# Optimization experiments

Measured on AMD Instinct MI355X. Metric: run time of the kernel, lower is better.

Reference implementation:

```python
import jax, jax.numpy as jnp
import numpy as np

SWIGLU_ALPHA = 1.702
SWIGLU_LIMIT = 7.0
B, S, H, E, K, I = 2, 2048, 2048, 32, 4, 1024


def setup_inputs() -> dict:
    key = jax.random.key(0)
    ks = jax.random.split(key, 8)
    return {
        "hidden_states": jax.random.normal(ks[0], (B, S, H), jnp.float32),
        "gate_w": jax.random.normal(ks[1], (E, H), jnp.float32) * 0.02,
        "gate_b": jnp.zeros((E,), jnp.float32),
        "w_gate": jax.random.normal(ks[2], (E, H, I), jnp.float32) * 0.02,
        "b_gate": jnp.zeros((E, I), jnp.float32),
        "w_up": jax.random.normal(ks[3], (E, H, I), jnp.float32) * 0.02,
        "b_up": jnp.zeros((E, I), jnp.float32),
        "w_down": jax.random.normal(ks[4], (E, I, H), jnp.float32) * 0.02,
        "b_down": jnp.zeros((E, H), jnp.float32),
    }


def reference(hidden_states, gate_w, gate_b, w_gate, b_gate, w_up, b_up, w_down, b_down):
    Bb, Ss, Hh = hidden_states.shape
    x = hidden_states.reshape(-1, Hh)                      # [T, H]
    # --- gate: top-k logits first, then softmax over the selected subset ---
    logits = x @ gate_w.T + gate_b                         # [T, E]
    topk_logits, topk_idx = jax.lax.top_k(logits, K)       # sorted descending
    topk_weight = jax.nn.softmax(topk_logits.astype(jnp.float32), axis=-1)  # [T, K]
    # --- dispatch: replicate each token K times, sort by expert id ---
    flat_idx = topk_idx.reshape(-1)                        # [T*K]
    xs = jnp.repeat(x, K, axis=0)                          # [T*K, H]
    order = jnp.argsort(flat_idx)                          # stable sort by expert
    xt = xs[order]
    gid = flat_idx[order]                                  # expert id per sorted row
    group_sizes = jnp.bincount(flat_idx, length=E).astype(jnp.int32)
    # --- grouped GEMM experts with GPT-OSS SwiGLU ---
    gate = jax.lax.ragged_dot(xt, w_gate, group_sizes) + b_gate[gid]
    up = jax.lax.ragged_dot(xt, w_up, group_sizes) + b_up[gid]
    gate = jnp.minimum(gate, SWIGLU_LIMIT)
    up = jnp.clip(up, -SWIGLU_LIMIT, SWIGLU_LIMIT)
    glu = gate * jax.nn.sigmoid(SWIGLU_ALPHA * gate)
    activated = (up + 1.0) * glu
    outs = jax.lax.ragged_dot(activated, w_down, group_sizes) + b_down[gid]
    # --- unsort and combine with routing weights ---
    inv = jnp.argsort(order)
    outs = outs[inv].reshape(-1, K, Hh)                    # [T, K, H]
    y = jnp.sum(outs * topk_weight[..., None], axis=1).astype(x.dtype)
    return y.reshape(Bb, Ss, Hh)
```

## Files before the change

### kernel.cpp

```cpp
#include <hip/hip_runtime.h>

#define T_TOK 4096
#define E_EXP 32
#define HDIM  2048
#define IDIM  1024
#define TKROW 16384
#define BM    256
#define MAXT  96

typedef __attribute__((ext_vector_type(8))) short   short8;
typedef __attribute__((ext_vector_type(8))) __bf16  bf16x8;
typedef __attribute__((ext_vector_type(4))) float   f32x4;

typedef const __attribute__((address_space(1))) unsigned int* gas_t;
typedef __attribute__((address_space(3))) unsigned int*       las_t;

static __device__ __forceinline__ void gload16(const void* g, void* l) {
    __builtin_amdgcn_global_load_lds((gas_t)(uintptr_t)g, (las_t)(uintptr_t)l, 16, 0, 0);
}

static __device__ __forceinline__ f32x4 mfma16(short8 a, short8 b, f32x4 c) {
    return __builtin_amdgcn_mfma_f32_16x16x32_bf16(
        __builtin_bit_cast(bf16x8, a), __builtin_bit_cast(bf16x8, b), c, 0, 0, 0);
}

static __device__ __forceinline__ unsigned short f2bf(float f) {
    unsigned u = __builtin_bit_cast(unsigned, f);
    unsigned r = (u + 0x7FFFu + ((u >> 16) & 1u)) >> 16;
    return (unsigned short)r;
}
static __device__ __forceinline__ float bf2f(unsigned short u) {
    return __builtin_bit_cast(float, ((unsigned)u) << 16);
}
static __device__ __forceinline__ unsigned cvtpk(float lo, float hi) {
    unsigned r;
    asm("v_cvt_pk_bf16_f32 %0, %1, %2" : "=v"(r) : "v"(lo), "v"(hi));
    return r;
}

#define VM0()   asm volatile("s_waitcnt vmcnt(0)" ::: "memory")
#define LGKM0() asm volatile("s_waitcnt lgkmcnt(0)" ::: "memory")

__global__ __launch_bounds__(256) void gating_kernel(
    const float* __restrict__ x, const float* __restrict__ gw,
    const float* __restrict__ gb, int* __restrict__ topk_idx,
    float* __restrict__ topk_w)
{
    int wave = threadIdx.x >> 6, lane = threadIdx.x & 63;
    int t = blockIdx.x * 4 + wave;
    const float* xr = x + (size_t)t * HDIM;
    float xv[32];
#pragma unroll
    for (int j = 0; j < 32; j++) xv[j] = xr[lane + 64 * j];
    float logits[E_EXP];
#pragma unroll
    for (int e = 0; e < E_EXP; e++) {
        const float* wr = gw + (size_t)e * HDIM;
        float s = 0.f;
#pragma unroll
        for (int j = 0; j < 32; j++) s = fmaf(xv[j], wr[lane + 64 * j], s);
#pragma unroll
        for (int off = 32; off; off >>= 1) s += __shfl_xor(s, off);
        logits[e] = s + gb[e];
    }
    unsigned sel = 0;
    float v[4]; int id[4];
#pragma unroll
    for (int kk = 0; kk < 4; kk++) {
        float best = -3.4e38f; int bi = 0;
#pragma unroll
        for (int e = 0; e < E_EXP; e++) {
            bool ok = ((sel >> e) & 1u) == 0u;
            bool gt = ok && (logits[e] > best);
            best = gt ? logits[e] : best;
            bi   = gt ? e : bi;
        }
        sel |= 1u << bi; v[kk] = best; id[kk] = bi;
    }
    float m0 = v[0];
    float e0 = __expf(v[0] - m0), e1 = __expf(v[1] - m0);
    float e2 = __expf(v[2] - m0), e3 = __expf(v[3] - m0);
    float inv = 1.f / (e0 + e1 + e2 + e3);
    if (lane == 0) {
        int b4 = t * 4;
        topk_idx[b4 + 0] = id[0]; topk_w[b4 + 0] = e0 * inv;
        topk_idx[b4 + 1] = id[1]; topk_w[b4 + 1] = e1 * inv;
        topk_idx[b4 + 2] = id[2]; topk_w[b4 + 2] = e2 * inv;
        topk_idx[b4 + 3] = id[3]; topk_w[b4 + 3] = e3 * inv;
    }
}

__global__ void init_kernel(int* counts, int* fill) {
    if (threadIdx.x < E_EXP) { counts[threadIdx.x] = 0; fill[threadIdx.x] = 0; }
}

__global__ void histo_kernel(const int* __restrict__ idx, int* counts) {
    int i = blockIdx.x * 256 + threadIdx.x;
    atomicAdd(&counts[idx[i]], 1);
}

__global__ void scan_tiles_kernel(const int* counts, int* offsets,
                                  int* tile_e, int* tile_r, int* ntiles) {
    if (threadIdx.x == 0) {
        int acc = 0;
        for (int e = 0; e < E_EXP; e++) { offsets[e] = acc; acc += counts[e]; }
        offsets[E_EXP] = acc;
        int nt = 0;
        for (int e = 0; e < E_EXP; e++) {
            int c = counts[e];
            for (int r = 0; r < c; r += BM) {
                tile_e[nt] = e; tile_r[nt] = offsets[e] + r; nt++;
            }
        }
        ntiles[0] = nt;
    }
}

__global__ void scatter_kernel(const int* __restrict__ idx, const int* __restrict__ offsets,
                               int* fill, int* __restrict__ pos_of, int* __restrict__ row_tok) {
    int i = blockIdx.x * 256 + threadIdx.x;
    int e = idx[i];
    int pos = offsets[e] + atomicAdd(&fill[e], 1);
    pos_of[i] = pos;
    row_tok[pos] = i >> 2;
}

__global__ __launch_bounds__(64) void gather_kernel(
    const float* __restrict__ x, const int* __restrict__ row_tok,
    unsigned short* __restrict__ xt)
{
    int r = blockIdx.x, lane = threadIdx.x;
    const f32x4* src = (const f32x4*)(x + (size_t)row_tok[r] * HDIM);
    unsigned short* dst = xt + (size_t)r * HDIM;
#pragma unroll
    for (int j = 0; j < 8; j++) {
        f32x4 f = src[lane + 64 * j];
        uint2 o;
        o.x = cvtpk(f[0], f[1]);
        o.y = cvtpk(f[2], f[3]);
        *(uint2*)(dst + 4 * (lane + 64 * j)) = o;
    }
}

__global__ __launch_bounds__(512, 2) void gemm1_kernel(
    const unsigned short* __restrict__ xt, const float* __restrict__ w_gate,
    const float* __restrict__ b_gate, const float* __restrict__ w_up,
    const float* __restrict__ b_up, const int* __restrict__ tile_e,
    const int* __restrict__ tile_r, const int* __restrict__ ntiles,
    const int* __restrict__ offsets, const int* __restrict__ counts,
    unsigned short* __restrict__ act)
{
    int flat = blockIdx.y * 8 + blockIdx.x;
    int swz = (flat & 7) * (MAXT * 8 / 8) + (flat >> 3);
    int tid = swz >> 3, nb = swz & 7;
    if (tid >= ntiles[0]) return;
    int e = tile_e[tid], row0 = tile_r[tid];
    int cnt_end = offsets[e] + counts[e];
    int n0 = nb * 128;

    __shared__ unsigned short As[2][BM * 64];
    __shared__ unsigned short Bgs[2][128 * 64];
    __shared__ unsigned short Bus[2][128 * 64];

    int t = threadIdx.x, lane = t & 63, w = t >> 6;
    int wr = w >> 2, wc = w & 3;
    int lrow = lane & 15, lg8 = (lane >> 4) * 8;

    f32x4 accg[8][2], accu[8][2];
#pragma unroll
    for (int m = 0; m < 8; m++)
#pragma unroll
        for (int n = 0; n < 2; n++) { accg[m][n] = (f32x4)0.f; accu[m][n] = (f32x4)0.f; }

    int arow_l = (lane >> 3);
    int achunk = (lane & 7) ^ arow_l;
    int bn = (t & 31) * 4, bk = (t >> 5) * 4;
    int bfswz = ((t & 31) & 7) << 3;
    size_t wB = (size_t)e * ((size_t)HDIM * IDIM) + (size_t)bk * IDIM + n0 + bn;

    f32x4 gReg[4], uReg[4];

#define G1_STAGE_A(KT, BUF) do { int k0_ = (KT) * 64; \
    _Pragma("unroll") for (int i_ = 0; i_ < 4; i_++) { \
        int ar_ = row0 + 32 * w + 8 * i_ + arow_l; \
        if (ar_ > TKROW - 1) ar_ = TKROW - 1; \
        gload16(xt + (size_t)ar_ * HDIM + k0_ + achunk * 8, \
                (void*)&As[BUF][(32 * w + 8 * i_) * 64]); \
    } } while (0)

#define G1_LOADB(KT) do { \
    const float* gp_ = w_gate + wB + (size_t)(KT) * 64 * IDIM; \
    const float* up_ = w_up   + wB + (size_t)(KT) * 64 * IDIM; \
    _Pragma("unroll") for (int kk_ = 0; kk_ < 4; kk_++) { \
        gReg[kk_] = *(const f32x4*)(gp_ + (size_t)kk_ * IDIM); \
        uReg[kk_] = *(const f32x4*)(up_ + (size_t)kk_ * IDIM); \
    } } while (0)

#define G1_WRITEB(BUF) do { \
    _Pragma("unroll") for (int j_ = 0; j_ < 4; j_++) { \
        uint2 vg_, vu_; \
        vg_.x = cvtpk(gReg[0][j_], gReg[1][j_]); vg_.y = cvtpk(gReg[2][j_], gReg[3][j_]); \
        vu_.x = cvtpk(uReg[0][j_], uReg[1][j_]); vu_.y = cvtpk(uReg[2][j_], uReg[3][j_]); \
        int d_ = (bn + j_) * 64 + (bk ^ bfswz); \
        *(uint2*)&Bgs[BUF][d_] = vg_; *(uint2*)&Bus[BUF][d_] = vu_; \
    } } while (0)

#define G1_MFMA(BUF) do { \
    __builtin_amdgcn_s_setprio(1); \
    _Pragma("unroll") for (int kk_ = 0; kk_ < 2; kk_++) { \
        short8 af_[8], bg_[2], bu_[2]; \
        int ke_ = kk_ * 32 + lg8; \
        _Pragma("unroll") for (int m_ = 0; m_ < 8; m_++) \
            af_[m_] = *(const short8*)&As[BUF][(wr * 128 + m_ * 16 + lrow) * 64 + (ke_ ^ ((lrow & 7) << 3))]; \
        _Pragma("unroll") for (int n_ = 0; n_ < 2; n_++) { \
            int rb_ = wc * 32 + n_ * 16 + lrow; \
            int d_ = rb_ * 64 + (ke_ ^ (((rb_ >> 2) & 7) << 3)); \
            bg_[n_] = *(const short8*)&Bgs[BUF][d_]; \
            bu_[n_] = *(const short8*)&Bus[BUF][d_]; \
        } \
        _Pragma("unroll") for (int m_ = 0; m_ < 8; m_++) \
        _Pragma("unroll") for (int n_ = 0; n_ < 2; n_++) { \
            accg[m_][n_] = mfma16(af_[m_], bg_[n_], accg[m_][n_]); \
            accu[m_][n_] = mfma16(af_[m_], bu_[n_], accu[m_][n_]); \
        } \
    } \
    __builtin_amdgcn_s_setprio(0); } while (0)

    G1_STAGE_A(0, 0);
    G1_LOADB(0);
    VM0();
    G1_WRITEB(0);
    LGKM0();
    __builtin_amdgcn_s_barrier();

    int cur = 0;
#pragma unroll 1
    for (int kt = 0; kt < 32; kt++) {
        if (kt + 1 < 32) { G1_STAGE_A(kt + 1, cur ^ 1); G1_LOADB(kt + 1); }
        G1_MFMA(cur);
        VM0();
        if (kt + 1 < 32) G1_WRITEB(cur ^ 1);
        LGKM0();
        __builtin_amdgcn_s_barrier();
        cur ^= 1;
    }
#undef G1_STAGE_A
#undef G1_LOADB
#undef G1_WRITEB
#undef G1_MFMA

#pragma unroll
    for (int nf = 0; nf < 2; nf++) {
        int col = n0 + wc * 32 + nf * 16 + lrow;
        float bgv = b_gate[e * IDIM + col];
        float buv = b_up[e * IDIM + col];
#pragma unroll
        for (int m = 0; m < 8; m++) {
            int rb = row0 + wr * 128 + m * 16 + (lane >> 4) * 4;
#pragma unroll
            for (int r = 0; r < 4; r++) {
                int grow = rb + r;
                if (grow < cnt_end) {
                    float gv = accg[m][nf][r] + bgv;
                    float uv = accu[m][nf][r] + buv;
                    gv = fminf(gv, 7.f);
                    uv = fminf(fmaxf(uv, -7.f), 7.f);
                    float glu = gv / (1.f + __expf(-1.702f * gv));
                    act[(size_t)grow * IDIM + col] = f2bf((uv + 1.f) * glu);
                }
            }
        }
    }
}

__global__ __launch_bounds__(512, 2) void gemm2_kernel(
    const unsigned short* __restrict__ actb, const float* __restrict__ w_down,
    const float* __restrict__ b_down, const int* __restrict__ tile_e,
    const int* __restrict__ tile_r, const int* __restrict__ ntiles,
    const int* __restrict__ offsets, const int* __restrict__ counts,
    unsigned short* __restrict__ outs)
{
    int flat = blockIdx.y * 8 + blockIdx.x;
    int swz = (flat & 7) * (MAXT * 8 / 8) + (flat >> 3);
    int tid = swz >> 3, nb = swz & 7;
    if (tid >= ntiles[0]) return;
    int e = tile_e[tid], row0 = tile_r[tid];
    int cnt_end = offsets[e] + counts[e];
    int n0 = nb * 256;

    __shared__ unsigned short As[2][BM * 64];
    __shared__ unsigned short Bs[2][256 * 64];

    int t = threadIdx.x, lane = t & 63, w = t >> 6;
    int wr = w >> 2, wc = w & 3;
    int lrow = lane & 15, lg8 = (lane >> 4) * 8;

    f32x4 acc[8][4];
#pragma unroll
    for (int m = 0; m < 8; m++)
#pragma unroll
        for (int n = 0; n < 4; n++) acc[m][n] = (f32x4)0.f;

    int arow_l = (lane >> 3);
    int achunk = (lane & 7) ^ arow_l;
    int bn = (t & 63) * 4, bk = w * 8;
    int bfswz = (lane & 7) << 3;
    size_t wB = (size_t)e * ((size_t)IDIM * HDIM) + (size_t)bk * HDIM + n0 + bn;

    f32x4 dReg[8];

#define G2_STAGE_A(KT, BUF) do { int k0_ = (KT) * 64; \
    _Pragma("unroll") for (int i_ = 0; i_ < 4; i_++) { \
        int ar_ = row0 + 32 * w + 8 * i_ + arow_l; \
        if (ar_ > TKROW - 1) ar_ = TKROW - 1; \
        gload16(actb + (size_t)ar_ * IDIM + k0_ + achunk * 8, \
                (void*)&As[BUF][(32 * w + 8 * i_) * 64]); \
    } } while (0)

#define G2_LOADB(KT) do { \
    const float* gp_ = w_down + wB + (size_t)(KT) * 64 * HDIM; \
    _Pragma("unroll") for (int kk_ = 0; kk_ < 8; kk_++) \
        dReg[kk_] = *(const f32x4*)(gp_ + (size_t)kk_ * HDIM); \
    } while (0)

#define G2_WRITEB(BUF) do { \
    _Pragma("unroll") for (int j_ = 0; j_ < 4; j_++) { \
        uint4 v_; \
        v_.x = cvtpk(dReg[0][j_], dReg[1][j_]); v_.y = cvtpk(dReg[2][j_], dReg[3][j_]); \
        v_.z = cvtpk(dReg[4][j_], dReg[5][j_]); v_.w = cvtpk(dReg[6][j_], dReg[7][j_]); \
        int d_ = (bn + j_) * 64 + (bk ^ bfswz); \
        *(uint4*)&Bs[BUF][d_] = v_; \
    } } while (0)

#define G2_MFMA(BUF) do { \
    __builtin_amdgcn_s_setprio(1); \
    _Pragma("unroll") for (int kk_ = 0; kk_ < 2; kk_++) { \
        short8 af_[8], bf_[4]; \
        int ke_ = kk_ * 32 + lg8; \
        _Pragma("unroll") for (int m_ = 0; m_ < 8; m_++) \
            af_[m_] = *(const short8*)&As[BUF][(wr * 128 + m_ * 16 + lrow) * 64 + (ke_ ^ ((lrow & 7) << 3))]; \
        _Pragma("unroll") for (int n_ = 0; n_ < 4; n_++) { \
            int rb_ = wc * 64 + n_ * 16 + lrow; \
            bf_[n_] = *(const short8*)&Bs[BUF][rb_ * 64 + (ke_ ^ (((rb_ >> 2) & 7) << 3))]; \
        } \
        _Pragma("unroll") for (int m_ = 0; m_ < 8; m_++) \
        _Pragma("unroll") for (int n_ = 0; n_ < 4; n_++) \
            acc[m_][n_] = mfma16(af_[m_], bf_[n_], acc[m_][n_]); \
    } \
    __builtin_amdgcn_s_setprio(0); } while (0)

    G2_STAGE_A(0, 0);
    G2_LOADB(0);
    VM0();
    G2_WRITEB(0);
    LGKM0();
    __builtin_amdgcn_s_barrier();

    int cur = 0;
#pragma unroll 1
    for (int kt = 0; kt < 16; kt++) {
        if (kt + 1 < 16) { G2_STAGE_A(kt + 1, cur ^ 1); G2_LOADB(kt + 1); }
        G2_MFMA(cur);
        VM0();
        if (kt + 1 < 16) G2_WRITEB(cur ^ 1);
        LGKM0();
        __builtin_amdgcn_s_barrier();
        cur ^= 1;
    }
#undef G2_STAGE_A
#undef G2_LOADB
#undef G2_WRITEB
#undef G2_MFMA

#pragma unroll
    for (int nf = 0; nf < 4; nf++) {
        int col = n0 + wc * 64 + nf * 16 + lrow;
        float bdv = b_down[e * HDIM + col];
#pragma unroll
        for (int m = 0; m < 8; m++) {
            int rb = row0 + wr * 128 + m * 16 + (lane >> 4) * 4;
#pragma unroll
            for (int r = 0; r < 4; r++) {
                int grow = rb + r;
                if (grow < cnt_end)
                    outs[(size_t)grow * HDIM + col] = f2bf(acc[m][nf][r] + bdv);
            }
        }
    }
}

__global__ __launch_bounds__(256) void combine_kernel(
    const unsigned short* __restrict__ outs, const int* __restrict__ pos_of,
    const float* __restrict__ topk_w, float* __restrict__ y)
{
    int tok = blockIdx.x;
    int c0 = threadIdx.x * 8;
    float acc[8] = {0.f, 0.f, 0.f, 0.f, 0.f, 0.f, 0.f, 0.f};
#pragma unroll
    for (int k = 0; k < 4; k++) {
        int pos = pos_of[tok * 4 + k];
        float w = topk_w[tok * 4 + k];
        short8 vv = *(const short8*)(outs + (size_t)pos * HDIM + c0);
#pragma unroll
        for (int j = 0; j < 8; j++)
            acc[j] = fmaf(w, bf2f((unsigned short)vv[j]), acc[j]);
    }
    float4 o0 = make_float4(acc[0], acc[1], acc[2], acc[3]);
    float4 o1 = make_float4(acc[4], acc[5], acc[6], acc[7]);
    *(float4*)(y + (size_t)tok * HDIM + c0)     = o0;
    *(float4*)(y + (size_t)tok * HDIM + c0 + 4) = o1;
}

extern "C" void kernel_launch(void* const* d_in, const int* in_sizes, int n_in,
                              void* d_out, int out_size, void* d_ws, size_t ws_size,
                              hipStream_t stream) {
    const float* x      = (const float*)d_in[0];
    const float* gw     = (const float*)d_in[1];
    const float* gb     = (const float*)d_in[2];
    const float* w_gate = (const float*)d_in[3];
    const float* b_gate = (const float*)d_in[4];
    const float* w_up   = (const float*)d_in[5];
    const float* b_up   = (const float*)d_in[6];
    const float* w_down = (const float*)d_in[7];
    const float* b_down = (const float*)d_in[8];
    float* y = (float*)d_out;

    char* base = (char*)d_ws;
    size_t off = 0;
    int*   topk_idx = (int*)(base + off);   off += (size_t)TKROW * 4;
    float* topk_w   = (float*)(base + off); off += (size_t)TKROW * 4;
    int*   counts   = (int*)(base + off);   off += 256;
    int*   offsets  = (int*)(base + off);   off += 256;
    int*   fill     = (int*)(base + off);   off += 256;
    int*   ntiles   = (int*)(base + off);   off += 256;
    int*   tile_e   = (int*)(base + off);   off += 1024;
    int*   tile_r   = (int*)(base + off);   off += 1024;
    int*   pos_of   = (int*)(base + off);   off += (size_t)TKROW * 4;
    int*   row_tok  = (int*)(base + off);   off += (size_t)TKROW * 4;
    unsigned short* xt   = (unsigned short*)(base + off); off += (size_t)TKROW * HDIM * 2;
    unsigned short* act  = (unsigned short*)(base + off); off += (size_t)TKROW * IDIM * 2;
    unsigned short* outs = (unsigned short*)(base + off); off += (size_t)TKROW * HDIM * 2;

    init_kernel<<<1, 64, 0, stream>>>(counts, fill);
    gating_kernel<<<T_TOK / 4, 256, 0, stream>>>(x, gw, gb, topk_idx, topk_w);
    histo_kernel<<<TKROW / 256, 256, 0, stream>>>(topk_idx, counts);
    scan_tiles_kernel<<<1, 64, 0, stream>>>(counts, offsets, tile_e, tile_r, ntiles);
    scatter_kernel<<<TKROW / 256, 256, 0, stream>>>(topk_idx, offsets, fill, pos_of, row_tok);
    gather_kernel<<<TKROW, 64, 0, stream>>>(x, row_tok, xt);
    gemm1_kernel<<<dim3(8, MAXT), 512, 0, stream>>>(
        xt, w_gate, b_gate, w_up, b_up, tile_e, tile_r, ntiles, offsets, counts, act);
    gemm2_kernel<<<dim3(8, MAXT), 512, 0, stream>>>(
        act, w_down, b_down, tile_e, tile_r, ntiles, offsets, counts, outs);
    combine_kernel<<<T_TOK, 256, 0, stream>>>(outs, pos_of, topk_w, y);
}
```

Measured before the change: 622.6 us.

## Stage fp32 expert weights directly to LDS and halve row tile size

Both grouped GEMMs now load fp32 weight tiles straight into shared memory with global_load_lds and convert them to bf16 while building MFMA fragments, replacing the register-staged load, convert and LDS write path. The M tile shrinks from 256 to 128 rows and the K step from 64 to 32, raising occupancy to 4 blocks per CU and reducing padding waste for ragged expert groups. In exchange, weights are read from LDS as scalar fp32 values with repeated conversion per wave, LDS traffic rises, and the tile count and barrier count double.

```diff
diff --git a/kernel.cpp b/kernel.cpp
--- a/kernel.cpp
+++ b/kernel.cpp
@@ -5,8 +5,8 @@
 #define HDIM  2048
 #define IDIM  1024
 #define TKROW 16384
-#define BM    256
-#define MAXT  96
+#define BM    128
+#define MAXT  160
 
 typedef __attribute__((ext_vector_type(8))) short   short8;
 typedef __attribute__((ext_vector_type(8))) __bf16  bf16x8;
@@ -37,9 +37,16 @@
     asm("v_cvt_pk_bf16_f32 %0, %1, %2" : "=v"(r) : "v"(lo), "v"(hi));
     return r;
 }
+static __device__ __forceinline__ short8 pack8(float v0, float v1, float v2, float v3,
+                                               float v4, float v5, float v6, float v7) {
+    uint4 u;
+    u.x = cvtpk(v0, v1); u.y = cvtpk(v2, v3);
+    u.z = cvtpk(v4, v5); u.w = cvtpk(v6, v7);
+    return __builtin_bit_cast(short8, u);
+}
 
 #define VM0()   asm volatile("s_waitcnt vmcnt(0)" ::: "memory")
-#define LGKM0() asm volatile("s_waitcnt lgkmcnt(0)" ::: "memory")
+#define BAR()   do { __builtin_amdgcn_s_barrier(); __builtin_amdgcn_sched_barrier(0); } while (0)
 
 __global__ __launch_bounds__(256) void gating_kernel(
     const float* __restrict__ x, const float* __restrict__ gw,
@@ -142,7 +149,7 @@
     }
 }
 
-__global__ __launch_bounds__(512, 2) void gemm1_kernel(
+__global__ __launch_bounds__(512, 4) void gemm1_kernel(
     const unsigned short* __restrict__ xt, const float* __restrict__ w_gate,
     const float* __restrict__ b_gate, const float* __restrict__ w_up,
     const float* __restrict__ b_up, const int* __restrict__ tile_e,
@@ -151,102 +158,80 @@
     unsigned short* __restrict__ act)
 {
     int flat = blockIdx.y * 8 + blockIdx.x;
-    int swz = (flat & 7) * (MAXT * 8 / 8) + (flat >> 3);
+    int swz = (flat & 7) * MAXT + (flat >> 3);
     int tid = swz >> 3, nb = swz & 7;
     if (tid >= ntiles[0]) return;
     int e = tile_e[tid], row0 = tile_r[tid];
     int cnt_end = offsets[e] + counts[e];
     int n0 = nb * 128;
 
-    __shared__ unsigned short As[2][BM * 64];
-    __shared__ unsigned short Bgs[2][128 * 64];
-    __shared__ unsigned short Bus[2][128 * 64];
+    __shared__ unsigned short As[2][BM * 32];
+    __shared__ float Bg[2][32 * 128];
+    __shared__ float Bu[2][32 * 128];
 
     int t = threadIdx.x, lane = t & 63, w = t >> 6;
     int wr = w >> 2, wc = w & 3;
-    int lrow = lane & 15, lg8 = (lane >> 4) * 8;
-
-    f32x4 accg[8][2], accu[8][2];
-#pragma unroll
-    for (int m = 0; m < 8; m++)
+    int lrow = lane & 15;
+    int kf8 = (lane >> 4) * 8;
+
+    f32x4 accg[4][2], accu[4][2];
+#pragma unroll
+    for (int m = 0; m < 4; m++)
 #pragma unroll
         for (int n = 0; n < 2; n++) { accg[m][n] = (f32x4)0.f; accu[m][n] = (f32x4)0.f; }
 
-    int arow_l = (lane >> 3);
-    int achunk = (lane & 7) ^ arow_l;
-    int bn = (t & 31) * 4, bk = (t >> 5) * 4;
-    int bfswz = ((t & 31) & 7) << 3;
-    size_t wB = (size_t)e * ((size_t)HDIM * IDIM) + (size_t)bk * IDIM + n0 + bn;
-
-    f32x4 gReg[4], uReg[4];
-
-#define G1_STAGE_A(KT, BUF) do { int k0_ = (KT) * 64; \
-    _Pragma("unroll") for (int i_ = 0; i_ < 4; i_++) { \
-        int ar_ = row0 + 32 * w + 8 * i_ + arow_l; \
-        if (ar_ > TKROW - 1) ar_ = TKROW - 1; \
-        gload16(xt + (size_t)ar_ * HDIM + k0_ + achunk * 8, \
-                (void*)&As[BUF][(32 * w + 8 * i_) * 64]); \
+    int arow = row0 + 16 * w + (lane >> 2);
+    if (arow > TKROW - 1) arow = TKROW - 1;
+    const unsigned short* aSrc = xt + (size_t)arow * HDIM + (lane & 3) * 8;
+    size_t eBase = (size_t)e * ((size_t)HDIM * IDIM);
+    const float* gSrc = w_gate + eBase + (size_t)(4 * w + (lane >> 5)) * IDIM + n0 + (lane & 31) * 4;
+    const float* uSrc = w_up   + eBase + (size_t)(4 * w + (lane >> 5)) * IDIM + n0 + (lane & 31) * 4;
+
+#define G1_STAGE(KT, BUF) do { \
+    gload16(aSrc + (size_t)(KT) * 32, (void*)&As[BUF][(16 * w) * 32]); \
+    _Pragma("unroll") for (int i_ = 0; i_ < 2; i_++) { \
+        size_t ko_ = (size_t)(KT) * 32 * IDIM + (size_t)(2 * i_) * IDIM; \
+        gload16(gSrc + ko_, (void*)&Bg[BUF][(4 * w + 2 * i_) * 128]); \
+        gload16(uSrc + ko_, (void*)&Bu[BUF][(4 * w + 2 * i_) * 128]); \
     } } while (0)
 
-#define G1_LOADB(KT) do { \
-    const float* gp_ = w_gate + wB + (size_t)(KT) * 64 * IDIM; \
-    const float* up_ = w_up   + wB + (size_t)(KT) * 64 * IDIM; \
-    _Pragma("unroll") for (int kk_ = 0; kk_ < 4; kk_++) { \
-        gReg[kk_] = *(const f32x4*)(gp_ + (size_t)kk_ * IDIM); \
-        uReg[kk_] = *(const f32x4*)(up_ + (size_t)kk_ * IDIM); \
-    } } while (0)
-
-#define G1_WRITEB(BUF) do { \
-    _Pragma("unroll") for (int j_ = 0; j_ < 4; j_++) { \
-        uint2 vg_, vu_; \
-        vg_.x = cvtpk(gReg[0][j_], gReg[1][j_]); vg_.y = cvtpk(gReg[2][j_], gReg[3][j_]); \
-        vu_.x = cvtpk(uReg[0][j_], uReg[1][j_]); vu_.y = cvtpk(uReg[2][j_], uReg[3][j_]); \
-        int d_ = (bn + j_) * 64 + (bk ^ bfswz); \
-        *(uint2*)&Bgs[BUF][d_] = vg_; *(uint2*)&Bus[BUF][d_] = vu_; \
-    } } while (0)
-
 #define G1_MFMA(BUF) do { \
+    const unsigned short* Ab_ = &As[BUF][0]; \
+    const float* Bgb_ = &Bg[BUF][0]; const float* Bub_ = &Bu[BUF][0]; \
+    short8 bgf_[2], buf_[2]; \
+    _Pragma("unroll") for (int nf_ = 0; nf_ < 2; nf_++) { \
+        int nc_ = wc * 32 + nf_ * 16 + lrow; \
+        bgf_[nf_] = pack8(Bgb_[(kf8 + 0) * 128 + nc_], Bgb_[(kf8 + 1) * 128 + nc_], \
+                          Bgb_[(kf8 + 2) * 128 + nc_], Bgb_[(kf8 + 3) * 128 + nc_], \
+                          Bgb_[(kf8 + 4) * 128 + nc_], Bgb_[(kf8 + 5) * 128 + nc_], \
+                          Bgb_[(kf8 + 6) * 128 + nc_], Bgb_[(kf8 + 7) * 128 + nc_]); \
+        buf_[nf_] = pack8(Bub_[(kf8 + 0) * 128 + nc_], Bub_[(kf8 + 1) * 128 + nc_], \
+                          Bub_[(kf8 + 2) * 128 + nc_], Bub_[(kf8 + 3) * 128 + nc_], \
+                          Bub_[(kf8 + 4) * 128 + nc_], Bub_[(kf8 + 5) * 128 + nc_], \
+                          Bub_[(kf8 + 6) * 128 + nc_], Bub_[(kf8 + 7) * 128 + nc_]); \
+    } \
     __builtin_amdgcn_s_setprio(1); \
-    _Pragma("unroll") for (int kk_ = 0; kk_ < 2; kk_++) { \
-        short8 af_[8], bg_[2], bu_[2]; \
-        int ke_ = kk_ * 32 + lg8; \
-        _Pragma("unroll") for (int m_ = 0; m_ < 8; m_++) \
-            af_[m_] = *(const short8*)&As[BUF][(wr * 128 + m_ * 16 + lrow) * 64 + (ke_ ^ ((lrow & 7) << 3))]; \
-        _Pragma("unroll") for (int n_ = 0; n_ < 2; n_++) { \
-            int rb_ = wc * 32 + n_ * 16 + lrow; \
-            int d_ = rb_ * 64 + (ke_ ^ (((rb_ >> 2) & 7) << 3)); \
-            bg_[n_] = *(const short8*)&Bgs[BUF][d_]; \
-            bu_[n_] = *(const short8*)&Bus[BUF][d_]; \
-        } \
-        _Pragma("unroll") for (int m_ = 0; m_ < 8; m_++) \
-        _Pragma("unroll") for (int n_ = 0; n_ < 2; n_++) { \
-            accg[m_][n_] = mfma16(af_[m_], bg_[n_], accg[m_][n_]); \
-            accu[m_][n_] = mfma16(af_[m_], bu_[n_], accu[m_][n_]); \
+    _Pragma("unroll") for (int m_ = 0; m_ < 4; m_++) { \
+        int rr_ = wr * 64 + m_ * 16 + lrow; \
+        short8 af_ = *(const short8*)&Ab_[rr_ * 32 + kf8]; \
+        _Pragma("unroll") for (int nf_ = 0; nf_ < 2; nf_++) { \
+            accg[m_][nf_] = mfma16(af_, bgf_[nf_], accg[m_][nf_]); \
+            accu[m_][nf_] = mfma16(af_, buf_[nf_], accu[m_][nf_]); \
         } \
     } \
     __builtin_amdgcn_s_setprio(0); } while (0)
 
-    G1_STAGE_A(0, 0);
-    G1_LOADB(0);
-    VM0();
-    G1_WRITEB(0);
-    LGKM0();
-    __builtin_amdgcn_s_barrier();
-
+    G1_STAGE(0, 0);
+    VM0(); BAR();
     int cur = 0;
 #pragma unroll 1
-    for (int kt = 0; kt < 32; kt++) {
-        if (kt + 1 < 32) { G1_STAGE_A(kt + 1, cur ^ 1); G1_LOADB(kt + 1); }
+    for (int kt = 0; kt < 64; kt++) {
+        if (kt + 1 < 64) G1_STAGE(kt + 1, cur ^ 1);
         G1_MFMA(cur);
-        VM0();
-        if (kt + 1 < 32) G1_WRITEB(cur ^ 1);
-        LGKM0();
-        __builtin_amdgcn_s_barrier();
+        VM0(); BAR();
         cur ^= 1;
     }
-#undef G1_STAGE_A
-#undef G1_LOADB
-#undef G1_WRITEB
+#undef G1_STAGE
 #undef G1_MFMA
 
 #pragma unroll
@@ -255,8 +240,8 @@
         float bgv = b_gate[e * IDIM + col];
         float buv = b_up[e * IDIM + col];
 #pragma unroll
-        for (int m = 0; m < 8; m++) {
-            int rb = row0 + wr * 128 + m * 16 + (lane >> 4) * 4;
+        for (int m = 0; m < 4; m++) {
+            int rb = row0 + wr * 64 + m * 16 + (lane >> 4) * 4;
 #pragma unroll
             for (int r = 0; r < 4; r++) {
                 int grow = rb + r;
@@ -273,7 +258,7 @@
     }
 }
 
-__global__ __launch_bounds__(512, 2) void gemm2_kernel(
+__global__ __launch_bounds__(512, 4) void gemm2_kernel(
     const unsigned short* __restrict__ actb, const float* __restrict__ w_down,
     const float* __restrict__ b_down, const int* __restrict__ tile_e,
     const int* __restrict__ tile_r, const int* __restrict__ ntiles,
@@ -281,95 +266,71 @@
     unsigned short* __restrict__ outs)
 {
     int flat = blockIdx.y * 8 + blockIdx.x;
-    int swz = (flat & 7) * (MAXT * 8 / 8) + (flat >> 3);
+    int swz = (flat & 7) * MAXT + (flat >> 3);
     int tid = swz >> 3, nb = swz & 7;
     if (tid >= ntiles[0]) return;
     int e = tile_e[tid], row0 = tile_r[tid];
     int cnt_end = offsets[e] + counts[e];
     int n0 = nb * 256;
 
-    __shared__ unsigned short As[2][BM * 64];
-    __shared__ unsigned short Bs[2][256 * 64];
+    __shared__ unsigned short As[2][BM * 32];
+    __shared__ float Bs[2][32 * 256];
 
     int t = threadIdx.x, lane = t & 63, w = t >> 6;
     int wr = w >> 2, wc = w & 3;
-    int lrow = lane & 15, lg8 = (lane >> 4) * 8;
-
-    f32x4 acc[8][4];
-#pragma unroll
-    for (int m = 0; m < 8; m++)
+    int lrow = lane & 15;
+    int kf8 = (lane >> 4) * 8;
+
+    f32x4 acc[4][4];
+#pragma unroll
+    for (int m = 0; m < 4; m++)
 #pragma unroll
         for (int n = 0; n < 4; n++) acc[m][n] = (f32x4)0.f;
 
-    int arow_l = (lane >> 3);
-    int achunk = (lane & 7) ^ arow_l;
-    int bn = (t & 63) * 4, bk = w * 8;
-    int bfswz = (lane & 7) << 3;
-    size_t wB = (size_t)e * ((size_t)IDIM * HDIM) + (size_t)bk * HDIM + n0 + bn;
-
-    f32x4 dReg[8];
-
-#define G2_STAGE_A(KT, BUF) do { int k0_ = (KT) * 64; \
+    int arow = row0 + 16 * w + (lane >> 2);
+    if (arow > TKROW - 1) arow = TKROW - 1;
+    const unsigned short* aSrc = actb + (size_t)arow * IDIM + (lane & 3) * 8;
+    const float* dSrc = w_down + (size_t)e * ((size_t)IDIM * HDIM)
+                        + (size_t)(4 * w) * HDIM + n0 + lane * 4;
+
+#define G2_STAGE(KT, BUF) do { \
+    gload16(aSrc + (size_t)(KT) * 32, (void*)&As[BUF][(16 * w) * 32]); \
     _Pragma("unroll") for (int i_ = 0; i_ < 4; i_++) { \
-        int ar_ = row0 + 32 * w + 8 * i_ + arow_l; \
-        if (ar_ > TKROW - 1) ar_ = TKROW - 1; \
-        gload16(actb + (size_t)ar_ * IDIM + k0_ + achunk * 8, \
-                (void*)&As[BUF][(32 * w + 8 * i_) * 64]); \
+        gload16(dSrc + (size_t)(KT) * 32 * HDIM + (size_t)i_ * HDIM, \
+                (void*)&Bs[BUF][(4 * w + i_) * 256]); \
     } } while (0)
 
-#define G2_LOADB(KT) do { \
-    const float* gp_ = w_down + wB + (size_t)(KT) * 64 * HDIM; \
-    _Pragma("unroll") for (int kk_ = 0; kk_ < 8; kk_++) \
-        dReg[kk_] = *(const f32x4*)(gp_ + (size_t)kk_ * HDIM); \
-    } while (0)
-
-#define G2_WRITEB(BUF) do { \
-    _Pragma("unroll") for (int j_ = 0; j_ < 4; j_++) { \
-        uint4 v_; \
-        v_.x = cvtpk(dReg[0][j_], dReg[1][j_]); v_.y = cvtpk(dReg[2][j_], dReg[3][j_]); \
-        v_.z = cvtpk(dReg[4][j_], dReg[5][j_]); v_.w = cvtpk(dReg[6][j_], dReg[7][j_]); \
-        int d_ = (bn + j_) * 64 + (bk ^ bfswz); \
-        *(uint4*)&Bs[BUF][d_] = v_; \
-    } } while (0)
-
 #define G2_MFMA(BUF) do { \
+    const unsigned short* Ab_ = &As[BUF][0]; \
+    const float* Bb_ = &Bs[BUF][0]; \
+    short8 bf_[4]; \
+    _Pragma("unroll") for (int nf_ = 0; nf_ < 4; nf_++) { \
+        int nc_ = wc * 64 + nf_ * 16 + lrow; \
+        bf_[nf_] = pack8(Bb_[(kf8 + 0) * 256 + nc_], Bb_[(kf8 + 1) * 256 + nc_], \
+                         Bb_[(kf8 + 2) * 256 + nc_], Bb_[(kf8 + 3) * 256 + nc_], \
+                         Bb_[(kf8 + 4) * 256 + nc_], Bb_[(kf8 + 5) * 256 + nc_], \
+                         Bb_[(kf8 + 6) * 256 + nc_], Bb_[(kf8 + 7) * 256 + nc_]); \
+    } \
     __builtin_amdgcn_s_setprio(1); \
-    _Pragma("unroll") for (int kk_ = 0; kk_ < 2; kk_++) { \
-        short8 af_[8], bf_[4]; \
-        int ke_ = kk_ * 32 + lg8; \
-        _Pragma("unroll") for (int m_ = 0; m_ < 8; m_++) \
-            af_[m_] = *(const short8*)&As[BUF][(wr * 128 + m_ * 16 + lrow) * 64 + (ke_ ^ ((lrow & 7) << 3))]; \
-        _Pragma("unroll") for (int n_ = 0; n_ < 4; n_++) { \
-            int rb_ = wc * 64 + n_ * 16 + lrow; \
-            bf_[n_] = *(const short8*)&Bs[BUF][rb_ * 64 + (ke_ ^ (((rb_ >> 2) & 7) << 3))]; \
-        } \
-        _Pragma("unroll") for (int m_ = 0; m_ < 8; m_++) \
-        _Pragma("unroll") for (int n_ = 0; n_ < 4; n_++) \
-            acc[m_][n_] = mfma16(af_[m_], bf_[n_], acc[m_][n_]); \
+    _Pragma("unroll") for (int m_ = 0; m_ < 4; m_++) { \
+        int rr_ = wr * 64 + m_ * 16 + lrow; \
+        short8 af_ = *(const short8*)&Ab_[rr_ * 32 + kf8]; \
+        _Pragma("unroll") for (int nf_ = 0; nf_ < 4; nf_++) \
+            acc[m_][nf_] = mfma16(af_, bf_[nf_], acc[m_][nf_]); \
     } \
     __builtin_amdgcn_s_setprio(0); } while (0)
 
-    G2_STAGE_A(0, 0);
-    G2_LOADB(0);
-    VM0();
-    G2_WRITEB(0);
-    LGKM0();
-    __builtin_amdgcn_s_barrier();
-
+    G2_STAGE(0, 0);
+    VM0(); BAR();
     int cur = 0;
 #pragma unroll 1
-    for (int kt = 0; kt < 16; kt++) {
-        if (kt + 1 < 16) { G2_STAGE_A(kt + 1, cur ^ 1); G2_LOADB(kt + 1); }
+    for (int kt = 0; kt < 32; kt++) {
+        if (kt + 1 < 32) G2_STAGE(kt + 1, cur ^ 1);
         G2_MFMA(cur);
-        VM0();
-        if (kt + 1 < 16) G2_WRITEB(cur ^ 1);
-        LGKM0();
-        __builtin_amdgcn_s_barrier();
+        VM0(); BAR();
         cur ^= 1;
     }
-#undef G2_STAGE_A
-#undef G2_LOADB
-#undef G2_WRITEB
+#undef G2_STAGE
 #undef G2_MFMA
 
 #pragma unroll
@@ -377,8 +338,8 @@
         int col = n0 + wc * 64 + nf * 16 + lrow;
         float bdv = b_down[e * HDIM + col];
 #pragma unroll
-        for (int m = 0; m < 8; m++) {
-            int rb = row0 + wr * 128 + m * 16 + (lane >> 4) * 4;
+        for (int m = 0; m < 4; m++) {
+            int rb = row0 + wr * 64 + m * 16 + (lane >> 4) * 4;
 #pragma unroll
             for (int r = 0; r < 4; r++) {
                 int grow = rb + r;
```

After: 668.4 us. 1.07x slower.

## Software-pipeline both expert GEMMs with split phases and halve gemm2 N-tile

Applied to the files above, without the earlier changes.

Both grouped GEMM kernels are restructured so each K-step is split into several barrier-separated phases that interleave LDS fragment reads, MFMA bursts, global prefetches and the bf16 conversion into shared memory. Weight registers are double-buffered two K-steps ahead, and partial vmcnt waits replace full drains. The intent is to hide global-load latency behind MFMA work instead of stalling each iteration. gemm2 also moves from 256-wide to 128-wide N tiles with twice the grid, which cuts per-block registers and LDS and adds parallelism, at the cost of reloading the A tile twice as often and paying more barriers per step.

```diff
diff --git a/kernel.cpp b/kernel.cpp
--- a/kernel.cpp
+++ b/kernel.cpp
@@ -38,8 +38,15 @@
     return r;
 }
 
-#define VM0()   asm volatile("s_waitcnt vmcnt(0)" ::: "memory")
-#define LGKM0() asm volatile("s_waitcnt lgkmcnt(0)" ::: "memory")
+#define FENCE()    asm volatile("" ::: "memory")
+#define WAITVM(N)  asm volatile("s_waitcnt vmcnt(" #N ")" ::: "memory")
+#define LGKM0()    asm volatile("s_waitcnt lgkmcnt(0)" ::: "memory")
+#define PHASE_SYNC() do { \
+    __builtin_amdgcn_s_barrier(); \
+    asm volatile("s_waitcnt lgkmcnt(0)" ::: "memory"); \
+    __builtin_amdgcn_sched_barrier(0); \
+} while (0)
+#define ENDP() do { __builtin_amdgcn_s_barrier(); __builtin_amdgcn_sched_barrier(0); } while (0)
 
 __global__ __launch_bounds__(256) void gating_kernel(
     const float* __restrict__ x, const float* __restrict__ gw,
@@ -151,7 +158,7 @@
     unsigned short* __restrict__ act)
 {
     int flat = blockIdx.y * 8 + blockIdx.x;
-    int swz = (flat & 7) * (MAXT * 8 / 8) + (flat >> 3);
+    int swz = (flat & 7) * 96 + (flat >> 3);
     int tid = swz >> 3, nb = swz & 7;
     if (tid >= ntiles[0]) return;
     int e = tile_e[tid], row0 = tile_r[tid];
@@ -178,7 +185,7 @@
     int bfswz = ((t & 31) & 7) << 3;
     size_t wB = (size_t)e * ((size_t)HDIM * IDIM) + (size_t)bk * IDIM + n0 + bn;
 
-    f32x4 gReg[4], uReg[4];
+    f32x4 gS0[4], uS0[4], gS1[4], uS1[4];
 
 #define G1_STAGE_A(KT, BUF) do { int k0_ = (KT) * 64; \
     _Pragma("unroll") for (int i_ = 0; i_ < 4; i_++) { \
@@ -188,66 +195,87 @@
                 (void*)&As[BUF][(32 * w + 8 * i_) * 64]); \
     } } while (0)
 
-#define G1_LOADB(KT) do { \
+#define G1_LOADB(KT, GV, UV) do { \
     const float* gp_ = w_gate + wB + (size_t)(KT) * 64 * IDIM; \
     const float* up_ = w_up   + wB + (size_t)(KT) * 64 * IDIM; \
     _Pragma("unroll") for (int kk_ = 0; kk_ < 4; kk_++) { \
-        gReg[kk_] = *(const f32x4*)(gp_ + (size_t)kk_ * IDIM); \
-        uReg[kk_] = *(const f32x4*)(up_ + (size_t)kk_ * IDIM); \
-    } } while (0)
-
-#define G1_WRITEB(BUF) do { \
+        GV[kk_] = *(const f32x4*)(gp_ + (size_t)kk_ * IDIM); \
+        UV[kk_] = *(const f32x4*)(up_ + (size_t)kk_ * IDIM); \
+    } } while (0)
+
+#define G1_WRITEB(GV, UV, BUF) do { \
     _Pragma("unroll") for (int j_ = 0; j_ < 4; j_++) { \
         uint2 vg_, vu_; \
-        vg_.x = cvtpk(gReg[0][j_], gReg[1][j_]); vg_.y = cvtpk(gReg[2][j_], gReg[3][j_]); \
-        vu_.x = cvtpk(uReg[0][j_], uReg[1][j_]); vu_.y = cvtpk(uReg[2][j_], uReg[3][j_]); \
+        vg_.x = cvtpk(GV[0][j_], GV[1][j_]); vg_.y = cvtpk(GV[2][j_], GV[3][j_]); \
+        vu_.x = cvtpk(UV[0][j_], UV[1][j_]); vu_.y = cvtpk(UV[2][j_], UV[3][j_]); \
         int d_ = (bn + j_) * 64 + (bk ^ bfswz); \
         *(uint2*)&Bgs[BUF][d_] = vg_; *(uint2*)&Bus[BUF][d_] = vu_; \
     } } while (0)
 
-#define G1_MFMA(BUF) do { \
+#define G1_RD_A(AF, CUR, MH, KK) do { \
+    _Pragma("unroll") for (int m_ = 0; m_ < 4; m_++) { \
+        int rr_ = wr * 128 + ((MH) * 4 + m_) * 16 + lrow; \
+        AF[m_] = *(const short8*)&As[CUR][rr_ * 64 + (((KK) * 32 + lg8) ^ ((lrow & 7) << 3))]; \
+    } } while (0)
+
+#define G1_RD_B(BG, BU, CUR, KK) do { \
+    _Pragma("unroll") for (int n_ = 0; n_ < 2; n_++) { \
+        int rb_ = wc * 32 + n_ * 16 + lrow; \
+        int d_ = rb_ * 64 + (((KK) * 32 + lg8) ^ (((rb_ >> 2) & 7) << 3)); \
+        BG[n_] = *(const short8*)&Bgs[CUR][d_]; \
+        BU[n_] = *(const short8*)&Bus[CUR][d_]; \
+    } } while (0)
+
+#define G1_MFMA16(AF, BG, BU, MH) do { \
     __builtin_amdgcn_s_setprio(1); \
-    _Pragma("unroll") for (int kk_ = 0; kk_ < 2; kk_++) { \
-        short8 af_[8], bg_[2], bu_[2]; \
-        int ke_ = kk_ * 32 + lg8; \
-        _Pragma("unroll") for (int m_ = 0; m_ < 8; m_++) \
-            af_[m_] = *(const short8*)&As[BUF][(wr * 128 + m_ * 16 + lrow) * 64 + (ke_ ^ ((lrow & 7) << 3))]; \
-        _Pragma("unroll") for (int n_ = 0; n_ < 2; n_++) { \
-            int rb_ = wc * 32 + n_ * 16 + lrow; \
-            int d_ = rb_ * 64 + (ke_ ^ (((rb_ >> 2) & 7) << 3)); \
-            bg_[n_] = *(const short8*)&Bgs[BUF][d_]; \
-            bu_[n_] = *(const short8*)&Bus[BUF][d_]; \
-        } \
-        _Pragma("unroll") for (int m_ = 0; m_ < 8; m_++) \
-        _Pragma("unroll") for (int n_ = 0; n_ < 2; n_++) { \
-            accg[m_][n_] = mfma16(af_[m_], bg_[n_], accg[m_][n_]); \
-            accu[m_][n_] = mfma16(af_[m_], bu_[n_], accu[m_][n_]); \
-        } \
+    _Pragma("unroll") for (int m_ = 0; m_ < 4; m_++) \
+    _Pragma("unroll") for (int n_ = 0; n_ < 2; n_++) { \
+        accg[(MH) * 4 + m_][n_] = mfma16(AF[m_], BG[n_], accg[(MH) * 4 + m_][n_]); \
+        accu[(MH) * 4 + m_][n_] = mfma16(AF[m_], BU[n_], accu[(MH) * 4 + m_][n_]); \
     } \
     __builtin_amdgcn_s_setprio(0); } while (0)
 
-    G1_STAGE_A(0, 0);
-    G1_LOADB(0);
-    VM0();
-    G1_WRITEB(0);
+#define G1_ITER(T, CUR, LG, LU, WG, WU) do { \
+    short8 af_[4], bg_[2], bu_[2]; \
+     \
+    G1_RD_A(af_, CUR, 0, 0); G1_RD_B(bg_, bu_, CUR, 0); \
+    if ((T) + 1 < 32) { FENCE(); G1_STAGE_A((T) + 1, (CUR) ^ 1); FENCE(); } \
+    PHASE_SYNC(); G1_MFMA16(af_, bg_, bu_, 0); ENDP(); \
+     \
+    G1_RD_A(af_, CUR, 1, 0); \
+    if ((T) + 2 < 32) { FENCE(); G1_LOADB((T) + 2, LG, LU); FENCE(); } \
+    PHASE_SYNC(); G1_MFMA16(af_, bg_, bu_, 1); ENDP(); \
+     \
+    G1_RD_A(af_, CUR, 0, 1); G1_RD_B(bg_, bu_, CUR, 1); \
+    if ((T) + 2 < 32) { WAITVM(12); } else if ((T) + 1 < 32) { WAITVM(4); } \
+    if ((T) + 1 < 32) G1_WRITEB(WG, WU, (CUR) ^ 1); \
+    PHASE_SYNC(); G1_MFMA16(af_, bg_, bu_, 0); ENDP(); \
+     \
+    G1_RD_A(af_, CUR, 1, 1); \
+    if ((T) + 2 < 32) { WAITVM(8); } else { WAITVM(0); } \
+    PHASE_SYNC(); G1_MFMA16(af_, bg_, bu_, 1); ENDP(); \
+} while (0)
+
+    G1_LOADB(0, gS0, uS0); FENCE();
+    G1_STAGE_A(0, 0); FENCE();
+    G1_LOADB(1, gS1, uS1); FENCE();
+    WAITVM(8);
+    G1_WRITEB(gS0, uS0, 0);
     LGKM0();
     __builtin_amdgcn_s_barrier();
 
-    int cur = 0;
 #pragma unroll 1
-    for (int kt = 0; kt < 32; kt++) {
-        if (kt + 1 < 32) { G1_STAGE_A(kt + 1, cur ^ 1); G1_LOADB(kt + 1); }
-        G1_MFMA(cur);
-        VM0();
-        if (kt + 1 < 32) G1_WRITEB(cur ^ 1);
-        LGKM0();
-        __builtin_amdgcn_s_barrier();
-        cur ^= 1;
+    for (int kt = 0; kt < 32; kt += 2) {
+        G1_ITER(kt,     0, gS0, uS0, gS1, uS1);
+        G1_ITER(kt + 1, 1, gS1, uS1, gS0, uS0);
     }
 #undef G1_STAGE_A
 #undef G1_LOADB
 #undef G1_WRITEB
-#undef G1_MFMA
+#undef G1_RD_A
+#undef G1_RD_B
+#undef G1_MFMA16
+#undef G1_ITER
 
 #pragma unroll
     for (int nf = 0; nf < 2; nf++) {
@@ -280,34 +308,34 @@
     const int* __restrict__ offsets, const int* __restrict__ counts,
     unsigned short* __restrict__ outs)
 {
-    int flat = blockIdx.y * 8 + blockIdx.x;
-    int swz = (flat & 7) * (MAXT * 8 / 8) + (flat >> 3);
-    int tid = swz >> 3, nb = swz & 7;
+    int flat = blockIdx.y * 16 + blockIdx.x;
+    int swz = (flat & 7) * 192 + (flat >> 3);
+    int tid = swz >> 4, nb = swz & 15;
     if (tid >= ntiles[0]) return;
     int e = tile_e[tid], row0 = tile_r[tid];
     int cnt_end = offsets[e] + counts[e];
-    int n0 = nb * 256;
+    int n0 = nb * 128;
 
     __shared__ unsigned short As[2][BM * 64];
-    __shared__ unsigned short Bs[2][256 * 64];
+    __shared__ unsigned short Bs[2][128 * 64];
 
     int t = threadIdx.x, lane = t & 63, w = t >> 6;
     int wr = w >> 2, wc = w & 3;
     int lrow = lane & 15, lg8 = (lane >> 4) * 8;
 
-    f32x4 acc[8][4];
+    f32x4 acc[8][2];
 #pragma unroll
     for (int m = 0; m < 8; m++)
 #pragma unroll
-        for (int n = 0; n < 4; n++) acc[m][n] = (f32x4)0.f;
+        for (int n = 0; n < 2; n++) acc[m][n] = (f32x4)0.f;
 
     int arow_l = (lane >> 3);
     int achunk = (lane & 7) ^ arow_l;
-    int bn = (t & 63) * 4, bk = w * 8;
-    int bfswz = (lane & 7) << 3;
+    int bn = (t & 31) * 4, bk = (t >> 5) * 4;
+    int bfswz = ((t & 31) & 7) << 3;
     size_t wB = (size_t)e * ((size_t)IDIM * HDIM) + (size_t)bk * HDIM + n0 + bn;
 
-    f32x4 dReg[8];
+    f32x4 dS0[4], dS1[4];
 
 #define G2_STAGE_A(KT, BUF) do { int k0_ = (KT) * 64; \
     _Pragma("unroll") for (int i_ = 0; i_ < 4; i_++) { \
@@ -317,64 +345,78 @@
                 (void*)&As[BUF][(32 * w + 8 * i_) * 64]); \
     } } while (0)
 
-#define G2_LOADB(KT) do { \
+#define G2_LOADB(KT, DV) do { \
     const float* gp_ = w_down + wB + (size_t)(KT) * 64 * HDIM; \
-    _Pragma("unroll") for (int kk_ = 0; kk_ < 8; kk_++) \
-        dReg[kk_] = *(const f32x4*)(gp_ + (size_t)kk_ * HDIM); \
+    _Pragma("unroll") for (int kk_ = 0; kk_ < 4; kk_++) \
+        DV[kk_] = *(const f32x4*)(gp_ + (size_t)kk_ * HDIM); \
     } while (0)
 
-#define G2_WRITEB(BUF) do { \
+#define G2_WRITEB(DV, BUF) do { \
     _Pragma("unroll") for (int j_ = 0; j_ < 4; j_++) { \
-        uint4 v_; \
-        v_.x = cvtpk(dReg[0][j_], dReg[1][j_]); v_.y = cvtpk(dReg[2][j_], dReg[3][j_]); \
-        v_.z = cvtpk(dReg[4][j_], dReg[5][j_]); v_.w = cvtpk(dReg[6][j_], dReg[7][j_]); \
+        uint2 v_; \
+        v_.x = cvtpk(DV[0][j_], DV[1][j_]); v_.y = cvtpk(DV[2][j_], DV[3][j_]); \
         int d_ = (bn + j_) * 64 + (bk ^ bfswz); \
-        *(uint4*)&Bs[BUF][d_] = v_; \
-    } } while (0)
-
-#define G2_MFMA(BUF) do { \
+        *(uint2*)&Bs[BUF][d_] = v_; \
+    } } while (0)
+
+#define G2_RD_A(AF, CUR, KK) do { \
+    _Pragma("unroll") for (int m_ = 0; m_ < 8; m_++) { \
+        int rr_ = wr * 128 + m_ * 16 + lrow; \
+        AF[m_] = *(const short8*)&As[CUR][rr_ * 64 + (((KK) * 32 + lg8) ^ ((lrow & 7) << 3))]; \
+    } } while (0)
+
+#define G2_RD_B(BF, CUR, KK) do { \
+    _Pragma("unroll") for (int n_ = 0; n_ < 2; n_++) { \
+        int rb_ = wc * 32 + n_ * 16 + lrow; \
+        BF[n_] = *(const short8*)&Bs[CUR][rb_ * 64 + (((KK) * 32 + lg8) ^ (((rb_ >> 2) & 7) << 3))]; \
+    } } while (0)
+
+#define G2_MFMA16(AF, BF) do { \
     __builtin_amdgcn_s_setprio(1); \
-    _Pragma("unroll") for (int kk_ = 0; kk_ < 2; kk_++) { \
-        short8 af_[8], bf_[4]; \
-        int ke_ = kk_ * 32 + lg8; \
-        _Pragma("unroll") for (int m_ = 0; m_ < 8; m_++) \
-            af_[m_] = *(const short8*)&As[BUF][(wr * 128 + m_ * 16 + lrow) * 64 + (ke_ ^ ((lrow & 7) << 3))]; \
-        _Pragma("unroll") for (int n_ = 0; n_ < 4; n_++) { \
-            int rb_ = wc * 64 + n_ * 16 + lrow; \
-            bf_[n_] = *(const short8*)&Bs[BUF][rb_ * 64 + (ke_ ^ (((rb_ >> 2) & 7) << 3))]; \
-        } \
-        _Pragma("unroll") for (int m_ = 0; m_ < 8; m_++) \
-        _Pragma("unroll") for (int n_ = 0; n_ < 4; n_++) \
-            acc[m_][n_] = mfma16(af_[m_], bf_[n_], acc[m_][n_]); \
-    } \
+    _Pragma("unroll") for (int m_ = 0; m_ < 8; m_++) \
+    _Pragma("unroll") for (int n_ = 0; n_ < 2; n_++) \
+        acc[m_][n_] = mfma16(AF[m_], BF[n_], acc[m_][n_]); \
     __builtin_amdgcn_s_setprio(0); } while (0)
 
-    G2_STAGE_A(0, 0);
-    G2_LOADB(0);
-    VM0();
-    G2_WRITEB(0);
+#define G2_ITER(T, CUR, LD, WD) do { \
+    short8 af_[8], bf_[2]; \
+     \
+    G2_RD_A(af_, CUR, 0); G2_RD_B(bf_, CUR, 0); \
+    if ((T) + 1 < 16) { FENCE(); G2_STAGE_A((T) + 1, (CUR) ^ 1); FENCE(); } \
+    if ((T) + 2 < 16) { FENCE(); G2_LOADB((T) + 2, LD); FENCE(); } \
+    PHASE_SYNC(); G2_MFMA16(af_, bf_); ENDP(); \
+     \
+    G2_RD_A(af_, CUR, 1); G2_RD_B(bf_, CUR, 1); \
+    if ((T) + 2 < 16) { WAITVM(8); } else if ((T) + 1 < 16) { WAITVM(4); } \
+    if ((T) + 1 < 16) G2_WRITEB(WD, (CUR) ^ 1); \
+    if ((T) + 2 < 16) { WAITVM(4); } else { WAITVM(0); } \
+    PHASE_SYNC(); G2_MFMA16(af_, bf_); ENDP(); \
+} while (0)
+
+    G2_LOADB(0, dS0); FENCE();
+    G2_STAGE_A(0, 0); FENCE();
+    G2_LOADB(1, dS1); FENCE();
+    WAITVM(4);
+    G2_WRITEB(dS0, 0);
     LGKM0();
     __builtin_amdgcn_s_barrier();
 
-    int cur = 0;
 #pragma unroll 1
-    for (int kt = 0; kt < 16; kt++) {
-        if (kt + 1 < 16) { G2_STAGE_A(kt + 1, cur ^ 1); G2_LOADB(kt + 1); }
-        G2_MFMA(cur);
-        VM0();
-        if (kt + 1 < 16) G2_WRITEB(cur ^ 1);
-        LGKM0();
-        __builtin_amdgcn_s_barrier();
-        cur ^= 1;
+    for (int kt = 0; kt < 16; kt += 2) {
+        G2_ITER(kt,     0, dS0, dS1);
+        G2_ITER(kt + 1, 1, dS1, dS0);
     }
 #undef G2_STAGE_A
 #undef G2_LOADB
 #undef G2_WRITEB
-#undef G2_MFMA
-
-#pragma unroll
-    for (int nf = 0; nf < 4; nf++) {
-        int col = n0 + wc * 64 + nf * 16 + lrow;
+#undef G2_RD_A
+#undef G2_RD_B
+#undef G2_MFMA16
+#undef G2_ITER
+
+#pragma unroll
+    for (int nf = 0; nf < 2; nf++) {
+        int col = n0 + wc * 32 + nf * 16 + lrow;
         float bdv = b_down[e * HDIM + col];
 #pragma unroll
         for (int m = 0; m < 8; m++) {
@@ -449,7 +491,7 @@
     gather_kernel<<<TKROW, 64, 0, stream>>>(x, row_tok, xt);
     gemm1_kernel<<<dim3(8, MAXT), 512, 0, stream>>>(
         xt, w_gate, b_gate, w_up, b_up, tile_e, tile_r, ntiles, offsets, counts, act);
-    gemm2_kernel<<<dim3(8, MAXT), 512, 0, stream>>>(
+    gemm2_kernel<<<dim3(16, MAXT), 512, 0, stream>>>(
         act, w_down, b_down, tile_e, tile_r, ntiles, offsets, counts, outs);
     combine_kernel<<<T_TOK, 256, 0, stream>>>(outs, pos_of, topk_w, y);
 }
```

Measured after the change: 1.477 ms. +137.2%, slower.
